# Kernel optimization log

Hardware: AMD Instinct MI355X
Metric: run time of the kernel (lower is better)

## Reference

```python
import jax, jax.numpy as jnp
import numpy as np

VOCAB = 100000
EMBED = 64
SENT = 20
MEM = 50
BATCH = 32
HOPS = 3
PAD_ID = 0


def position_encoding(sentence_size, embedding_size):
    # Section 4.1 of MemN2N paper, vectorized. Returns [sentence_size, embedding_size].
    i = np.arange(1, embedding_size + 1, dtype=np.float32)[:, None]   # [E,1]
    j = np.arange(1, sentence_size + 1, dtype=np.float32)[None, :]    # [1,S]
    enc = (i - (embedding_size + 1) / 2.0) * (j - (sentence_size + 1) / 2.0)
    enc = 1.0 + 4.0 * enc / embedding_size / sentence_size
    enc[:, -1] = 1.0
    return jnp.asarray(enc.T, dtype=jnp.float32)  # [S,E]


def setup_inputs() -> dict:
    key = jax.random.key(0)
    k1, k2, k3, k4 = jax.random.split(key, 4)
    stories = jax.random.randint(k1, (BATCH, MEM, SENT), 0, VOCAB, dtype=jnp.int64 if jax.config.jax_enable_x64 else jnp.int32)
    queries = jax.random.randint(k2, (BATCH, SENT), 0, VOCAB, dtype=jnp.int64 if jax.config.jax_enable_x64 else jnp.int32)
    A = jax.random.normal(k3, (VOCAB, EMBED), dtype=jnp.float32) * 0.1
    C = jax.random.normal(k4, (HOPS, VOCAB, EMBED), dtype=jnp.float32) * 0.1
    # padding_idx=PAD_ID rows are zero, as in nn.Embedding(padding_idx=...)
    A = A.at[PAD_ID].set(0.0)
    C = C.at[:, PAD_ID].set(0.0)
    encoding = position_encoding(SENT, EMBED)
    return {"stories": stories, "queries": queries, "A": A, "C": C, "encoding": encoding}


def reference(stories, queries, A, C, encoding):
    # queries: [B,S], stories: [B,M,S], A: [V,E], C: [hops,V,E], encoding: [S,E]
    q_emb = A[queries]                                # [B,S,E]
    u = (q_emb * encoding).sum(axis=1)                # [B,E]
    for hop in range(HOPS):
        table_in = A if hop == 0 else C[hop - 1]
        emb_A = table_in[stories]                     # [B,M,S,E]
        m = (emb_A * encoding).sum(axis=2)            # [B,M,E]
        dotted = jnp.einsum('bme,be->bm', m, u)       # [B,M]
        probs = jax.nn.softmax(dotted, axis=-1)       # [B,M]
        emb_C = C[hop][stories]                       # [B,M,S,E]
        c = (emb_C * encoding).sum(axis=2)            # [B,M,E]
        o = jnp.einsum('bm,bme->be', probs, c)        # [B,E]
        u = u + o
    return u @ C[-1].T                                # [B,V]
```

## Files before the change

### kernel.cpp

```cpp
#include <hip/hip_runtime.h>
#include <hip/hip_bf16.h>

#define VOCAB 100000
#define EMBED 64
#define SENT  20
#define MEM   50
#define BATCH 32
#define HOPS  3

#define NSET  4
#define NSLOT (NSET * BATCH * MEM)

__device__ __forceinline__ float bfr(unsigned short x) {
    union { unsigned int u; float f; } cv;
    cv.u = ((unsigned int)x) << 16;
    return cv.f;
}

__device__ __forceinline__ bool is_bf16(const void* enc) {
    return ((const unsigned int*)enc)[639] == 0x3F803F80u;
}

__device__ __forceinline__ float loadT(const void* p, size_t idx, bool bf) {
    return bf ? bfr(((const unsigned short*)p)[idx]) : ((const float*)p)[idx];
}

__device__ __forceinline__ float wave_sum(float d) {
#pragma unroll
    for (int off = 32; off > 0; off >>= 1) d += __shfl_xor(d, off, 64);
    return d;
}

__global__ __launch_bounds__(256) void k_gather(
    const int* __restrict__ stories,
    const int* __restrict__ queries,
    const void* __restrict__ A,
    const void* __restrict__ C,
    const void* __restrict__ enc,
    float* __restrict__ mc_ws,
    float* __restrict__ u0g)
{
    const bool bf = is_bf16(enc);
    const int tid = threadIdx.x;
    const int e   = tid & 63;
    const int gw  = blockIdx.x * 4 + (tid >> 6);
    const size_t VE = (size_t)VOCAB * EMBED;

    float encr[SENT];
#pragma unroll
    for (int s = 0; s < SENT; ++s) encr[s] = loadT(enc, s * EMBED + e, bf);

    if (gw < NSLOT) {
        const int t  = gw / (BATCH * MEM);
        const int bm = gw % (BATCH * MEM);
        const void* T   = (t == 0) ? A : C;
        const size_t to = (t == 0) ? 0 : (size_t)(t - 1) * VE;

        int wst = (e < SENT) ? stories[bm * SENT + e] : 0;
        float acc = 0.f;
#pragma unroll
        for (int s = 0; s < SENT; ++s) {
            int w = __shfl(wst, s, 64);
            acc += loadT(T, to + (size_t)w * EMBED + e, bf) * encr[s];
        }
        mc_ws[gw * EMBED + e] = acc;
    } else if (gw < NSLOT + BATCH) {
        const int b = gw - NSLOT;
        int wq = (e < SENT) ? queries[b * SENT + e] : 0;
        float u = 0.f;
#pragma unroll
        for (int s = 0; s < SENT; ++s) {
            int w = __shfl(wq, s, 64);
            u += loadT(A, (size_t)w * EMBED + e, bf) * encr[s];
        }
        u0g[b * EMBED + e] = u;
    }
}

__global__ __launch_bounds__(256) void k_recur2(
    const float* __restrict__ mc_ws,
    const float* __restrict__ u0g,
    float* __restrict__ u3g)
{
    const int b    = blockIdx.x;
    const int tid  = threadIdx.x;
    const int lane = tid & 63;
    const int widx = tid >> 6;

    __shared__ float mc[NSET][MEM][65];
    __shared__ float uls[EMBED];
    __shared__ float ols[4][EMBED];

    for (int idx = tid; idx < NSET * MEM * 16; idx += 256) {
        int t  = idx / (MEM * 16);
        int r  = idx % (MEM * 16);
        int mm = r >> 4;
        int e4 = r & 15;
        const float4 v = *(const float4*)(mc_ws +
            (((size_t)t * BATCH * MEM) + (size_t)b * MEM + mm) * EMBED + e4 * 4);
        mc[t][mm][e4 * 4 + 0] = v.x;
        mc[t][mm][e4 * 4 + 1] = v.y;
        mc[t][mm][e4 * 4 + 2] = v.z;
        mc[t][mm][e4 * 4 + 3] = v.w;
    }
    if (tid < EMBED) uls[tid] = u0g[b * EMBED + tid];
    __syncthreads();

    for (int hop = 0; hop < HOPS; ++hop) {
        float d = 0.f;
        if (lane < MEM) {
#pragma unroll
            for (int e = 0; e < EMBED; ++e)
                d += mc[hop][lane][e] * uls[e];
        }
        float x = (lane < MEM) ? d : -3.4e38f;
        float mx = x;
#pragma unroll
        for (int off = 32; off > 0; off >>= 1) mx = fmaxf(mx, __shfl_xor(mx, off, 64));
        float ex = (lane < MEM) ? __expf(x - mx) : 0.f;
        float sm = wave_sum(ex);
        float p = ex / sm;

        float o = 0.f;
#pragma unroll
        for (int k = 0; k < 13; ++k) {
            int mm = widx * 13 + k;
            if (mm < MEM)
                o += __shfl(p, mm, 64) * mc[hop + 1][mm][lane];
        }
        ols[widx][lane] = o;
        __syncthreads();
        if (tid < EMBED)
            uls[tid] += ols[0][tid] + ols[1][tid] + ols[2][tid] + ols[3][tid];
        __syncthreads();
    }

    if (tid < EMBED) u3g[b * EMBED + tid] = uls[tid];
}

__global__ __launch_bounds__(256) void k_out(const float* __restrict__ u,
                                             const void* __restrict__ Cbase,
                                             const void* __restrict__ enc,
                                             void* __restrict__ out)
{
    bool bf = is_bf16(enc);
    const size_t c2_off = (size_t)2 * VOCAB * EMBED;
    __shared__ __align__(16) float su[BATCH * EMBED];
    for (int i = threadIdx.x; i < BATCH * EMBED; i += 256) su[i] = u[i];
    __syncthreads();
    int v = blockIdx.x * 256 + threadIdx.x;
    if (v >= VOCAB) return;

    float row[EMBED];
    if (bf) {
        const uint4* rp = (const uint4*)((const unsigned short*)Cbase + c2_off + (size_t)v * EMBED);
#pragma unroll
        for (int i = 0; i < 8; ++i) {
            uint4 r = rp[i];
            row[i*8 + 0] = bfr((unsigned short)(r.x & 0xffff));
            row[i*8 + 1] = bfr((unsigned short)(r.x >> 16));
            row[i*8 + 2] = bfr((unsigned short)(r.y & 0xffff));
            row[i*8 + 3] = bfr((unsigned short)(r.y >> 16));
            row[i*8 + 4] = bfr((unsigned short)(r.z & 0xffff));
            row[i*8 + 5] = bfr((unsigned short)(r.z >> 16));
            row[i*8 + 6] = bfr((unsigned short)(r.w & 0xffff));
            row[i*8 + 7] = bfr((unsigned short)(r.w >> 16));
        }
    } else {
        const float4* rp = (const float4*)((const float*)Cbase + c2_off + (size_t)v * EMBED);
#pragma unroll
        for (int i = 0; i < 16; ++i) {
            float4 r = rp[i];
            row[i*4 + 0] = r.x; row[i*4 + 1] = r.y;
            row[i*4 + 2] = r.z; row[i*4 + 3] = r.w;
        }
    }

    float res[BATCH];
#pragma unroll
    for (int bb = 0; bb < BATCH; ++bb) {
        const float4* sp = (const float4*)(su + bb * EMBED);
        float acc = 0.f;
#pragma unroll
        for (int e4 = 0; e4 < 16; ++e4) {
            float4 us = sp[e4];
            acc += row[e4*4+0]*us.x + row[e4*4+1]*us.y
                 + row[e4*4+2]*us.z + row[e4*4+3]*us.w;
        }
        res[bb] = acc;
    }

    if (bf) {
        unsigned short* ob = (unsigned short*)out;
#pragma unroll
        for (int bb = 0; bb < BATCH; ++bb) {
            __hip_bfloat16 h = __float2bfloat16(res[bb]);
            ob[(size_t)bb * VOCAB + v] = *(unsigned short*)&h;
        }
    } else {
        float* of = (float*)out;
#pragma unroll
        for (int bb = 0; bb < BATCH; ++bb)
            of[(size_t)bb * VOCAB + v] = res[bb];
    }
}

extern "C" void kernel_launch(void* const* d_in, const int* in_sizes, int n_in,
                              void* d_out, int out_size, void* d_ws, size_t ws_size,
                              hipStream_t stream)
{
    const int*  stories = (const int*)d_in[0];
    const int*  queries = (const int*)d_in[1];
    const void* A       = d_in[2];
    const void* C       = d_in[3];
    const void* enc     = d_in[4];

    float* mc_ws = (float*)d_ws;
    float* u0g   = mc_ws + NSLOT * EMBED;
    float* u3g   = u0g + BATCH * EMBED;

    const int nwaves  = NSLOT + BATCH;
    const int nblocks = (nwaves + 3) / 4;

    k_gather<<<nblocks, 256, 0, stream>>>(stories, queries, A, C, enc, mc_ws, u0g);
    k_recur2<<<BATCH, 256, 0, stream>>>(mc_ws, u0g, u3g);
    k_out<<<(VOCAB + 255) / 256, 256, 0, stream>>>(u3g, C, enc, d_out);
}
```

Baseline: 159.0 us.

## Fuse embedding gather and hop recurrence into one per-batch kernel

Merges the gather and recurrence kernels into a single 1024-thread block per batch element that gathers memory embeddings straight into LDS. This removes one kernel launch and the workspace round trip through global memory. It also templates the bf16/fp32 paths so the dtype branch is resolved at compile time. The trade-off is that the gather now runs on only 32 blocks, which limits parallelism for the latency-bound random row loads.

```diff
diff --git a/kernel.cpp b/kernel.cpp
--- a/kernel.cpp
+++ b/kernel.cpp
@@ -8,8 +8,9 @@
 #define BATCH 32
 #define HOPS  3
 
-#define NSET  4
-#define NSLOT (NSET * BATCH * MEM)
+#define NSET   4
+#define NSLOTB (NSET * MEM)
+#define LDSP   65
 
 __device__ __forceinline__ float bfr(unsigned short x) {
     union { unsigned int u; float f; } cv;
@@ -21,8 +22,10 @@
     return ((const unsigned int*)enc)[639] == 0x3F803F80u;
 }
 
-__device__ __forceinline__ float loadT(const void* p, size_t idx, bool bf) {
-    return bf ? bfr(((const unsigned short*)p)[idx]) : ((const float*)p)[idx];
+template<bool BF>
+__device__ __forceinline__ float ldT(const void* p, size_t idx) {
+    if constexpr (BF) return bfr(((const unsigned short*)p)[idx]);
+    else              return ((const float*)p)[idx];
 }
 
 __device__ __forceinline__ float wave_sum(float d) {
@@ -31,104 +34,102 @@
     return d;
 }
 
-__global__ __launch_bounds__(256) void k_gather(
+template<bool BF>
+__device__ __forceinline__ void gather_all(const int* __restrict__ stories,
+                                           const int* __restrict__ queries,
+                                           const void* __restrict__ A,
+                                           const void* __restrict__ C,
+                                           const void* __restrict__ enc,
+                                           float* __restrict__ mc,
+                                           float* __restrict__ uls,
+                                           int b)
+{
+    const int tid = threadIdx.x;
+    const int e   = tid & 63;
+    const int w   = tid >> 6;
+    const size_t VE = (size_t)VOCAB * EMBED;
+
+    float encr[SENT];
+#pragma unroll
+    for (int s = 0; s < SENT; ++s) encr[s] = ldT<BF>(enc, s * EMBED + e);
+
+    for (int slot = w; slot < NSLOTB + 1; slot += 16) {
+        if (slot < NSLOTB) {
+            const int t  = slot / MEM;
+            const int mm = slot % MEM;
+            const void* T   = (t == 0) ? A : C;
+            const size_t to = (t == 0) ? 0 : (size_t)(t - 1) * VE;
+
+            int wst = (e < SENT) ? stories[(b * MEM + mm) * SENT + e] : 0;
+            float acc = 0.f;
+#pragma unroll
+            for (int s = 0; s < SENT; ++s) {
+                int wd = __shfl(wst, s, 64);
+                acc += ldT<BF>(T, to + (size_t)wd * EMBED + e) * encr[s];
+            }
+            mc[(t * MEM + mm) * LDSP + e] = acc;
+        } else {
+            int wq = (e < SENT) ? queries[b * SENT + e] : 0;
+            float u = 0.f;
+#pragma unroll
+            for (int s = 0; s < SENT; ++s) {
+                int wd = __shfl(wq, s, 64);
+                u += ldT<BF>(A, (size_t)wd * EMBED + e) * encr[s];
+            }
+            uls[e] = u;
+        }
+    }
+}
+
+__global__ __launch_bounds__(1024) void k_front(
     const int* __restrict__ stories,
     const int* __restrict__ queries,
     const void* __restrict__ A,
     const void* __restrict__ C,
     const void* __restrict__ enc,
-    float* __restrict__ mc_ws,
-    float* __restrict__ u0g)
-{
+    float* __restrict__ u3g)
+{
+    __shared__ float mc[NSET * MEM * LDSP];
+    __shared__ float uls[EMBED];
+    __shared__ float ols[4][EMBED];
+
     const bool bf = is_bf16(enc);
+    const int b   = blockIdx.x;
     const int tid = threadIdx.x;
-    const int e   = tid & 63;
-    const int gw  = blockIdx.x * 4 + (tid >> 6);
-    const size_t VE = (size_t)VOCAB * EMBED;
-
-    float encr[SENT];
-#pragma unroll
-    for (int s = 0; s < SENT; ++s) encr[s] = loadT(enc, s * EMBED + e, bf);
-
-    if (gw < NSLOT) {
-        const int t  = gw / (BATCH * MEM);
-        const int bm = gw % (BATCH * MEM);
-        const void* T   = (t == 0) ? A : C;
-        const size_t to = (t == 0) ? 0 : (size_t)(t - 1) * VE;
-
-        int wst = (e < SENT) ? stories[bm * SENT + e] : 0;
-        float acc = 0.f;
-#pragma unroll
-        for (int s = 0; s < SENT; ++s) {
-            int w = __shfl(wst, s, 64);
-            acc += loadT(T, to + (size_t)w * EMBED + e, bf) * encr[s];
-        }
-        mc_ws[gw * EMBED + e] = acc;
-    } else if (gw < NSLOT + BATCH) {
-        const int b = gw - NSLOT;
-        int wq = (e < SENT) ? queries[b * SENT + e] : 0;
-        float u = 0.f;
-#pragma unroll
-        for (int s = 0; s < SENT; ++s) {
-            int w = __shfl(wq, s, 64);
-            u += loadT(A, (size_t)w * EMBED + e, bf) * encr[s];
-        }
-        u0g[b * EMBED + e] = u;
-    }
-}
-
-__global__ __launch_bounds__(256) void k_recur2(
-    const float* __restrict__ mc_ws,
-    const float* __restrict__ u0g,
-    float* __restrict__ u3g)
-{
-    const int b    = blockIdx.x;
-    const int tid  = threadIdx.x;
+
+    if (bf) gather_all<true >(stories, queries, A, C, enc, mc, uls, b);
+    else    gather_all<false>(stories, queries, A, C, enc, mc, uls, b);
+    __syncthreads();
+
     const int lane = tid & 63;
     const int widx = tid >> 6;
 
-    __shared__ float mc[NSET][MEM][65];
-    __shared__ float uls[EMBED];
-    __shared__ float ols[4][EMBED];
-
-    for (int idx = tid; idx < NSET * MEM * 16; idx += 256) {
-        int t  = idx / (MEM * 16);
-        int r  = idx % (MEM * 16);
-        int mm = r >> 4;
-        int e4 = r & 15;
-        const float4 v = *(const float4*)(mc_ws +
-            (((size_t)t * BATCH * MEM) + (size_t)b * MEM + mm) * EMBED + e4 * 4);
-        mc[t][mm][e4 * 4 + 0] = v.x;
-        mc[t][mm][e4 * 4 + 1] = v.y;
-        mc[t][mm][e4 * 4 + 2] = v.z;
-        mc[t][mm][e4 * 4 + 3] = v.w;
-    }
-    if (tid < EMBED) uls[tid] = u0g[b * EMBED + tid];
-    __syncthreads();
-
     for (int hop = 0; hop < HOPS; ++hop) {
-        float d = 0.f;
-        if (lane < MEM) {
-#pragma unroll
-            for (int e = 0; e < EMBED; ++e)
-                d += mc[hop][lane][e] * uls[e];
-        }
-        float x = (lane < MEM) ? d : -3.4e38f;
-        float mx = x;
-#pragma unroll
-        for (int off = 32; off > 0; off >>= 1) mx = fmaxf(mx, __shfl_xor(mx, off, 64));
-        float ex = (lane < MEM) ? __expf(x - mx) : 0.f;
-        float sm = wave_sum(ex);
-        float p = ex / sm;
-
-        float o = 0.f;
-#pragma unroll
-        for (int k = 0; k < 13; ++k) {
-            int mm = widx * 13 + k;
-            if (mm < MEM)
-                o += __shfl(p, mm, 64) * mc[hop + 1][mm][lane];
-        }
-        ols[widx][lane] = o;
+        if (tid < 256) {
+            float d = 0.f;
+            if (lane < MEM) {
+                const float* row = mc + (hop * MEM + lane) * LDSP;
+#pragma unroll
+                for (int e2 = 0; e2 < EMBED; ++e2) d += row[e2] * uls[e2];
+            }
+            float x  = (lane < MEM) ? d : -3.4e38f;
+            float mx = x;
+#pragma unroll
+            for (int off = 32; off > 0; off >>= 1) mx = fmaxf(mx, __shfl_xor(mx, off, 64));
+            float ex = (lane < MEM) ? __expf(x - mx) : 0.f;
+            float sm = wave_sum(ex);
+            float p  = ex / sm;
+
+            float o = 0.f;
+            const float* crow = mc + ((hop + 1) * MEM) * LDSP;
+#pragma unroll
+            for (int k = 0; k < 13; ++k) {
+                int mm = widx * 13 + k;
+                if (mm < MEM)
+                    o += __shfl(p, mm, 64) * crow[mm * LDSP + lane];
+            }
+            ols[widx][lane] = o;
+        }
         __syncthreads();
         if (tid < EMBED)
             uls[tid] += ols[0][tid] + ols[1][tid] + ols[2][tid] + ols[3][tid];
@@ -138,21 +139,14 @@
     if (tid < EMBED) u3g[b * EMBED + tid] = uls[tid];
 }
 
-__global__ __launch_bounds__(256) void k_out(const float* __restrict__ u,
-                                             const void* __restrict__ Cbase,
-                                             const void* __restrict__ enc,
-                                             void* __restrict__ out)
-{
-    bool bf = is_bf16(enc);
+template<bool BF>
+__device__ __forceinline__ void out_one(const float* __restrict__ su,
+                                        const void* __restrict__ Cbase,
+                                        void* __restrict__ out, int v)
+{
     const size_t c2_off = (size_t)2 * VOCAB * EMBED;
-    __shared__ __align__(16) float su[BATCH * EMBED];
-    for (int i = threadIdx.x; i < BATCH * EMBED; i += 256) su[i] = u[i];
-    __syncthreads();
-    int v = blockIdx.x * 256 + threadIdx.x;
-    if (v >= VOCAB) return;
-
     float row[EMBED];
-    if (bf) {
+    if constexpr (BF) {
         const uint4* rp = (const uint4*)((const unsigned short*)Cbase + c2_off + (size_t)v * EMBED);
 #pragma unroll
         for (int i = 0; i < 8; ++i) {
@@ -190,7 +184,7 @@
         res[bb] = acc;
     }
 
-    if (bf) {
+    if constexpr (BF) {
         unsigned short* ob = (unsigned short*)out;
 #pragma unroll
         for (int bb = 0; bb < BATCH; ++bb) {
@@ -203,6 +197,21 @@
         for (int bb = 0; bb < BATCH; ++bb)
             of[(size_t)bb * VOCAB + v] = res[bb];
     }
+}
+
+__global__ __launch_bounds__(256) void k_out(const float* __restrict__ u,
+                                             const void* __restrict__ Cbase,
+                                             const void* __restrict__ enc,
+                                             void* __restrict__ out)
+{
+    const bool bf = is_bf16(enc);
+    __shared__ __align__(16) float su[BATCH * EMBED];
+    for (int i = threadIdx.x; i < BATCH * EMBED; i += 256) su[i] = u[i];
+    __syncthreads();
+    const int v = blockIdx.x * 256 + threadIdx.x;
+    if (v >= VOCAB) return;
+    if (bf) out_one<true >(su, Cbase, enc ? out : out, v);
+    else    out_one<false>(su, Cbase, out, v);
 }
 
 extern "C" void kernel_launch(void* const* d_in, const int* in_sizes, int n_in,
@@ -215,14 +224,8 @@
     const void* C       = d_in[3];
     const void* enc     = d_in[4];
 
-    float* mc_ws = (float*)d_ws;
-    float* u0g   = mc_ws + NSLOT * EMBED;
-    float* u3g   = u0g + BATCH * EMBED;
-
-    const int nwaves  = NSLOT + BATCH;
-    const int nblocks = (nwaves + 3) / 4;
-
-    k_gather<<<nblocks, 256, 0, stream>>>(stories, queries, A, C, enc, mc_ws, u0g);
-    k_recur2<<<BATCH, 256, 0, stream>>>(mc_ws, u0g, u3g);
+    float* u3g = (float*)d_ws;
+
+    k_front<<<BATCH, 1024, 0, stream>>>(stories, queries, A, C, enc, u3g);
     k_out<<<(VOCAB + 255) / 256, 256, 0, stream>>>(u3g, C, enc, d_out);
 }
```

Result: slower. 169.7 us (+6.7%).
